# Kernel tuning notes

Measured on AMD Instinct MI355X. Metric: run time of the kernel, lower is better.

Reference implementation:

```python
import jax, jax.numpy as jnp
import numpy as np

HSIZE = 128
E = 640000


def _init_linear(key, fan_in, fan_out):
    # torch nn.Linear default init: U(-1/sqrt(fan_in), 1/sqrt(fan_in))
    kw, kb = jax.random.split(key)
    bound = 1.0 / np.sqrt(fan_in)
    W = jax.random.uniform(kw, (fan_in, fan_out), jnp.float32, -bound, bound)
    b = jax.random.uniform(kb, (fan_out,), jnp.float32, -bound, bound)
    return W, b


def setup_inputs() -> dict:
    key = jax.random.key(0)
    ks = jax.random.split(key, 6)
    hself = jax.random.normal(ks[0], (E, HSIZE), jnp.float32)
    hother = jax.random.normal(ks[1], (E, HSIZE), jnp.float32)
    Wm1, bm1 = _init_linear(ks[2], 2 * HSIZE, HSIZE)
    Wm2, bm2 = _init_linear(ks[3], HSIZE, HSIZE)
    Wu1, bu1 = _init_linear(ks[4], 2 * HSIZE, HSIZE)
    Wu2, bu2 = _init_linear(ks[5], HSIZE, HSIZE)
    return {"hself": hself, "hother": hother,
            "Wm1": Wm1, "bm1": bm1, "Wm2": Wm2, "bm2": bm2,
            "Wu1": Wu1, "bu1": bu1, "Wu2": Wu2, "bu2": bu2}


def _mlp2(a, b, W1, b1, W2, b2):
    # concat([a, b], -1) @ W1 done without materializing the concat
    h = a @ W1[:HSIZE] + b @ W1[HSIZE:] + b1
    h = jax.nn.relu(h)
    return h @ W2 + b2


def reference(hself, hother, Wm1, bm1, Wm2, bm2, Wu1, bu1, Wu2, bu2):
    # msg: Linear(2h,h) -> ReLU -> Linear(h,h) on cat([hself, hother])
    msg = _mlp2(hself, hother, Wm1, bm1, Wm2, bm2)
    # upd: Linear(2h,h) -> ReLU -> Linear(h,h) on cat([hself, msg])
    out = _mlp2(hself, msg, Wu1, bu1, Wu2, bu2)
    return out
```

## Files before the change

### kernel.cpp

```cpp
#include <hip/hip_runtime.h>

typedef __bf16 bf16_t;
typedef __bf16 bf16x8 __attribute__((ext_vector_type(8)));
typedef float f32x4 __attribute__((ext_vector_type(4)));

#define MFMA(a, b, c) __builtin_amdgcn_mfma_f32_16x16x32_bf16((a), (b), (c), 0, 0, 0)

#define E_ROWS 640000
#define BM 256

static __device__ __forceinline__ bf16x8 cvt8(float4 a, float4 b) {
  bf16x8 r;
  r[0] = (bf16_t)a.x; r[1] = (bf16_t)a.y; r[2] = (bf16_t)a.z; r[3] = (bf16_t)a.w;
  r[4] = (bf16_t)b.x; r[5] = (bf16_t)b.y; r[6] = (bf16_t)b.z; r[7] = (bf16_t)b.w;
  return r;
}

static __device__ __forceinline__ unsigned int pk2(float a, float b) {
  unsigned short ua = __builtin_bit_cast(unsigned short, (bf16_t)a);
  unsigned short ub = __builtin_bit_cast(unsigned short, (bf16_t)b);
  return ((unsigned int)ub << 16) | ua;
}

static __device__ __forceinline__ void gload_lds16(const void* g, void* l) {
  __builtin_amdgcn_global_load_lds(
      (const __attribute__((address_space(1))) unsigned int*)g,
      (__attribute__((address_space(3))) unsigned int*)l, 16, 0, 0);
}

__global__ __launch_bounds__(256) void prep_weights(
    const float* __restrict__ Wm1, const float* __restrict__ Wm2,
    const float* __restrict__ Wu1, const float* __restrict__ Wu2,
    bf16_t* __restrict__ wt) {
  int c = blockIdx.x * 256 + threadIdx.x;
  if (c >= 12288) return;
  int lane = c & 63, f = c >> 6;
  const float* W; int base;
  if (f < 64)       { W = Wm1; base = 0;   }
  else if (f < 96)  { W = Wm2; base = 64;  }
  else if (f < 160) { W = Wu1; base = 96;  }
  else              { W = Wu2; base = 160; }
  int fl = f - base;
  int ks = fl >> 3, nb = fl & 7;
  int k0 = 32 * ks + 8 * (lane >> 4);
  int n  = 16 * nb + (lane & 15);
  bf16x8 v;
  #pragma unroll
  for (int j = 0; j < 8; ++j) v[j] = (bf16_t)W[(size_t)(k0 + j) * 128 + n];
  ((bf16x8*)wt)[c] = v;
}

#define STAGE96(tc0) { \
  _Pragma("unroll") \
  for (int i_ = 0; i_ < 12; ++i_) \
    gload_lds16((const char*)wt + ((size_t)((tc0) + i_ * 512 + tid)) * 16, \
                smem + (i_ * 512 + tid) * 16); }

#define LDW8(s, base, fl0) \
  s##0 = *(const bf16x8*)((base) + ((fl0) + 0) * 1024 + lane * 16); \
  s##1 = *(const bf16x8*)((base) + ((fl0) + 1) * 1024 + lane * 16); \
  s##2 = *(const bf16x8*)((base) + ((fl0) + 2) * 1024 + lane * 16); \
  s##3 = *(const bf16x8*)((base) + ((fl0) + 3) * 1024 + lane * 16); \
  s##4 = *(const bf16x8*)((base) + ((fl0) + 4) * 1024 + lane * 16); \
  s##5 = *(const bf16x8*)((base) + ((fl0) + 5) * 1024 + lane * 16); \
  s##6 = *(const bf16x8*)((base) + ((fl0) + 6) * 1024 + lane * 16); \
  s##7 = *(const bf16x8*)((base) + ((fl0) + 7) * 1024 + lane * 16);

#define ROUND(s, x0, x1) \
  acc00 = MFMA(s##0, x0, acc00); acc10 = MFMA(s##0, x1, acc10); \
  acc01 = MFMA(s##1, x0, acc01); acc11 = MFMA(s##1, x1, acc11); \
  acc02 = MFMA(s##2, x0, acc02); acc12 = MFMA(s##2, x1, acc12); \
  acc03 = MFMA(s##3, x0, acc03); acc13 = MFMA(s##3, x1, acc13); \
  acc04 = MFMA(s##4, x0, acc04); acc14 = MFMA(s##4, x1, acc14); \
  acc05 = MFMA(s##5, x0, acc05); acc15 = MFMA(s##5, x1, acc15); \
  acc06 = MFMA(s##6, x0, acc06); acc16 = MFMA(s##6, x1, acc16); \
  acc07 = MFMA(s##7, x0, acc07); acc17 = MFMA(s##7, x1, acc17);

#define ACCINIT(bp) { const float* bp_ = (bp) + g * 4; float4 q; \
  q = *(const float4*)(bp_ +   0); acc00 = (f32x4){q.x,q.y,q.z,q.w}; acc10 = acc00; \
  q = *(const float4*)(bp_ +  16); acc01 = (f32x4){q.x,q.y,q.z,q.w}; acc11 = acc01; \
  q = *(const float4*)(bp_ +  32); acc02 = (f32x4){q.x,q.y,q.z,q.w}; acc12 = acc02; \
  q = *(const float4*)(bp_ +  48); acc03 = (f32x4){q.x,q.y,q.z,q.w}; acc13 = acc03; \
  q = *(const float4*)(bp_ +  64); acc04 = (f32x4){q.x,q.y,q.z,q.w}; acc14 = acc04; \
  q = *(const float4*)(bp_ +  80); acc05 = (f32x4){q.x,q.y,q.z,q.w}; acc15 = acc05; \
  q = *(const float4*)(bp_ +  96); acc06 = (f32x4){q.x,q.y,q.z,q.w}; acc16 = acc06; \
  q = *(const float4*)(bp_ + 112); acc07 = (f32x4){q.x,q.y,q.z,q.w}; acc17 = acc07; }

#define RPK_H(av, nb, R) { \
  f32x4 v = av; \
  float e0 = v[0], e1 = v[1], e2 = v[2], e3 = v[3]; \
  if (R) { e0 = fmaxf(e0, 0.f); e1 = fmaxf(e1, 0.f); \
           e2 = fmaxf(e2, 0.f); e3 = fmaxf(e3, 0.f); } \
  uint2 w; w.x = pk2(e0, e1); w.y = pk2(e2, e3); \
  int dl = c + 16 * (2 * ((nb) & 1) + (g >> 1)); \
  *(uint2*)(myrep + (((nb) >> 1) * 64 + dl) * 16 + (g & 1) * 8) = w; }

#define WAITLDS asm volatile("s_waitcnt lgkmcnt(0)" ::: "memory");
#define VMCNT0  asm volatile("s_waitcnt vmcnt(0)" ::: "memory");

#define REPACK(R) \
  RPK_H(acc00, 0, R) RPK_H(acc01, 1, R) RPK_H(acc02, 2, R) RPK_H(acc03, 3, R) \
  RPK_H(acc04, 4, R) RPK_H(acc05, 5, R) RPK_H(acc06, 6, R) RPK_H(acc07, 7, R) \
  WAITLDS \
  x00 = *(const bf16x8*)(myrep + (0 * 64 + lane) * 16); \
  x01 = *(const bf16x8*)(myrep + (1 * 64 + lane) * 16); \
  x02 = *(const bf16x8*)(myrep + (2 * 64 + lane) * 16); \
  x03 = *(const bf16x8*)(myrep + (3 * 64 + lane) * 16); \
  WAITLDS \
  RPK_H(acc10, 0, R) RPK_H(acc11, 1, R) RPK_H(acc12, 2, R) RPK_H(acc13, 3, R) \
  RPK_H(acc14, 4, R) RPK_H(acc15, 5, R) RPK_H(acc16, 6, R) RPK_H(acc17, 7, R) \
  WAITLDS \
  x10 = *(const bf16x8*)(myrep + (0 * 64 + lane) * 16); \
  x11 = *(const bf16x8*)(myrep + (1 * 64 + lane) * 16); \
  x12 = *(const bf16x8*)(myrep + (2 * 64 + lane) * 16); \
  x13 = *(const bf16x8*)(myrep + (3 * 64 + lane) * 16); \
  WAITLDS

#define LOADX(d0, d1, basep, kk) { \
  float4 a0 = *(const float4*)((basep) + r0 + (kk) * 32); \
  float4 a1 = *(const float4*)((basep) + r0 + (kk) * 32 + 4); \
  float4 b0 = *(const float4*)((basep) + r1 + (kk) * 32); \
  float4 b1 = *(const float4*)((basep) + r1 + (kk) * 32 + 4); \
  d0 = cvt8(a0, a1); d1 = cvt8(b0, b1); }

#define ST(av, mt, nb) { f32x4 v = av; \
  *(float4*)(out + (rowbase + (mt) * 16 + c) * 128 + (nb) * 16 + g * 4) = \
      (float4){v[0], v[1], v[2], v[3]}; }

__global__ __launch_bounds__(512) void fused_mp(
    const float* __restrict__ hself, const float* __restrict__ hother,
    const bf16_t* __restrict__ wt,
    const float* __restrict__ bm1, const float* __restrict__ bm2,
    const float* __restrict__ bu1, const float* __restrict__ bu2,
    float* __restrict__ out) {
  __shared__ char smem[131072];

  const int tid = threadIdx.x;
  const int lane = tid & 63;
  const int wave = tid >> 6;
  const int c = lane & 15;
  const int g = lane >> 4;

  char* W1 = smem;
  char* W2 = smem + 65536;
  char* myrep = smem + 98304 + wave * 4096;

  const size_t rowbase = (size_t)blockIdx.x * BM + wave * 32;
  const size_t r0 = (rowbase + c) * 128 + g * 8;
  const size_t r1 = (rowbase + 16 + c) * 128 + g * 8;

  bf16x8 hs00, hs01, hs02, hs03, hs10, hs11, hs12, hs13;
  bf16x8 x00, x01, x02, x03, x10, x11, x12, x13;
  LOADX(hs00, hs10, hself, 0)
  LOADX(hs01, hs11, hself, 1)
  LOADX(hs02, hs12, hself, 2)
  LOADX(hs03, hs13, hself, 3)
  STAGE96(0)
  LOADX(x00, x10, hother, 0)
  LOADX(x01, x11, hother, 1)
  LOADX(x02, x12, hother, 2)
  LOADX(x03, x13, hother, 3)
  VMCNT0
  __syncthreads();

  f32x4 acc00, acc01, acc02, acc03, acc04, acc05, acc06, acc07;
  f32x4 acc10, acc11, acc12, acc13, acc14, acc15, acc16, acc17;
  bf16x8 wa0, wa1, wa2, wa3, wa4, wa5, wa6, wa7;

  ACCINIT(bm1)
  LDW8(wa, W1, 0)   ROUND(wa, hs00, hs10)
  LDW8(wa, W1, 8)   ROUND(wa, hs01, hs11)
  LDW8(wa, W1, 16)  ROUND(wa, hs02, hs12)
  LDW8(wa, W1, 24)  ROUND(wa, hs03, hs13)
  LDW8(wa, W1, 32)  ROUND(wa, x00, x10)
  LDW8(wa, W1, 40)  ROUND(wa, x01, x11)
  LDW8(wa, W1, 48)  ROUND(wa, x02, x12)
  LDW8(wa, W1, 56)  ROUND(wa, x03, x13)

  REPACK(true)

  ACCINIT(bm2)
  LDW8(wa, W2, 0)   ROUND(wa, x00, x10)
  LDW8(wa, W2, 8)   ROUND(wa, x01, x11)
  LDW8(wa, W2, 16)  ROUND(wa, x02, x12)
  LDW8(wa, W2, 24)  ROUND(wa, x03, x13)

  REPACK(false)

  __syncthreads();
  STAGE96(6144)
  VMCNT0
  __syncthreads();

  ACCINIT(bu1)
  LDW8(wa, W1, 0)   ROUND(wa, hs00, hs10)
  LDW8(wa, W1, 8)   ROUND(wa, hs01, hs11)
  LDW8(wa, W1, 16)  ROUND(wa, hs02, hs12)
  LDW8(wa, W1, 24)  ROUND(wa, hs03, hs13)
  LDW8(wa, W1, 32)  ROUND(wa, x00, x10)
  LDW8(wa, W1, 40)  ROUND(wa, x01, x11)
  LDW8(wa, W1, 48)  ROUND(wa, x02, x12)
  LDW8(wa, W1, 56)  ROUND(wa, x03, x13)

  REPACK(true)

  ACCINIT(bu2)
  LDW8(wa, W2, 0)   ROUND(wa, x00, x10)
  LDW8(wa, W2, 8)   ROUND(wa, x01, x11)
  LDW8(wa, W2, 16)  ROUND(wa, x02, x12)
  LDW8(wa, W2, 24)  ROUND(wa, x03, x13)

  ST(acc00, 0, 0) ST(acc01, 0, 1) ST(acc02, 0, 2) ST(acc03, 0, 3)
  ST(acc04, 0, 4) ST(acc05, 0, 5) ST(acc06, 0, 6) ST(acc07, 0, 7)
  ST(acc10, 1, 0) ST(acc11, 1, 1) ST(acc12, 1, 2) ST(acc13, 1, 3)
  ST(acc14, 1, 4) ST(acc15, 1, 5) ST(acc16, 1, 6) ST(acc17, 1, 7)
}

extern "C" void kernel_launch(void* const* d_in, const int* in_sizes, int n_in,
                              void* d_out, int out_size, void* d_ws, size_t ws_size,
                              hipStream_t stream) {
  const float* hself  = (const float*)d_in[0];
  const float* hother = (const float*)d_in[1];
  const float* Wm1 = (const float*)d_in[2];
  const float* bm1 = (const float*)d_in[3];
  const float* Wm2 = (const float*)d_in[4];
  const float* bm2 = (const float*)d_in[5];
  const float* Wu1 = (const float*)d_in[6];
  const float* bu1 = (const float*)d_in[7];
  const float* Wu2 = (const float*)d_in[8];
  const float* bu2 = (const float*)d_in[9];
  float* out = (float*)d_out;
  bf16_t* wt = (bf16_t*)d_ws;

  prep_weights<<<48, 256, 0, stream>>>(Wm1, Wm2, Wu1, Wu2, wt);
  fused_mp<<<E_ROWS / BM, 512, 0, stream>>>(hself, hother, wt,
                                            bm1, bm2, bu1, bu2, out);
}
```

Before: 289.2 us.

## Make fused MLP kernel persistent with double-buffered prefetch of next tile

The kernel becomes persistent: 250 blocks each loop over 10 row tiles in two interleaved register sets (A/B). The next tile's hother and hself loads and the weight restaging are issued before the current tile's compute and waited on with partial vmcnt, so global latency can overlap MFMA work. This removes per-block launch and prologue costs, but it doubles input register pressure and issues a redundant final prefetch (tile index wraps to 0). With 250 blocks on a 256-CU part, load balance and occupancy may suffer.

```diff
diff --git a/kernel.cpp b/kernel.cpp
--- a/kernel.cpp
+++ b/kernel.cpp
@@ -8,6 +8,8 @@
 
 #define E_ROWS 640000
 #define BM 256
+#define NTILE 2500
+#define GRID 250
 
 static __device__ __forceinline__ bf16x8 cvt8(float4 a, float4 b) {
   bf16x8 r;
@@ -97,35 +99,81 @@
 
 #define WAITLDS asm volatile("s_waitcnt lgkmcnt(0)" ::: "memory");
 #define VMCNT0  asm volatile("s_waitcnt vmcnt(0)" ::: "memory");
-
-#define REPACK(R) \
+#define VMCNT16 asm volatile("s_waitcnt vmcnt(16)" ::: "memory");
+
+#define REPACK(R, x) \
   RPK_H(acc00, 0, R) RPK_H(acc01, 1, R) RPK_H(acc02, 2, R) RPK_H(acc03, 3, R) \
   RPK_H(acc04, 4, R) RPK_H(acc05, 5, R) RPK_H(acc06, 6, R) RPK_H(acc07, 7, R) \
   WAITLDS \
-  x00 = *(const bf16x8*)(myrep + (0 * 64 + lane) * 16); \
-  x01 = *(const bf16x8*)(myrep + (1 * 64 + lane) * 16); \
-  x02 = *(const bf16x8*)(myrep + (2 * 64 + lane) * 16); \
-  x03 = *(const bf16x8*)(myrep + (3 * 64 + lane) * 16); \
+  x##00 = *(const bf16x8*)(myrep + (0 * 64 + lane) * 16); \
+  x##01 = *(const bf16x8*)(myrep + (1 * 64 + lane) * 16); \
+  x##02 = *(const bf16x8*)(myrep + (2 * 64 + lane) * 16); \
+  x##03 = *(const bf16x8*)(myrep + (3 * 64 + lane) * 16); \
   WAITLDS \
   RPK_H(acc10, 0, R) RPK_H(acc11, 1, R) RPK_H(acc12, 2, R) RPK_H(acc13, 3, R) \
   RPK_H(acc14, 4, R) RPK_H(acc15, 5, R) RPK_H(acc16, 6, R) RPK_H(acc17, 7, R) \
   WAITLDS \
-  x10 = *(const bf16x8*)(myrep + (0 * 64 + lane) * 16); \
-  x11 = *(const bf16x8*)(myrep + (1 * 64 + lane) * 16); \
-  x12 = *(const bf16x8*)(myrep + (2 * 64 + lane) * 16); \
-  x13 = *(const bf16x8*)(myrep + (3 * 64 + lane) * 16); \
+  x##10 = *(const bf16x8*)(myrep + (0 * 64 + lane) * 16); \
+  x##11 = *(const bf16x8*)(myrep + (1 * 64 + lane) * 16); \
+  x##12 = *(const bf16x8*)(myrep + (2 * 64 + lane) * 16); \
+  x##13 = *(const bf16x8*)(myrep + (3 * 64 + lane) * 16); \
   WAITLDS
 
-#define LOADX(d0, d1, basep, kk) { \
-  float4 a0 = *(const float4*)((basep) + r0 + (kk) * 32); \
-  float4 a1 = *(const float4*)((basep) + r0 + (kk) * 32 + 4); \
-  float4 b0 = *(const float4*)((basep) + r1 + (kk) * 32); \
-  float4 b1 = *(const float4*)((basep) + r1 + (kk) * 32 + 4); \
+#define LOADX(d0, d1, basep, kk, rr0, rr1) { \
+  float4 a0 = *(const float4*)((basep) + (rr0) + (kk) * 32); \
+  float4 a1 = *(const float4*)((basep) + (rr0) + (kk) * 32 + 4); \
+  float4 b0 = *(const float4*)((basep) + (rr1) + (kk) * 32); \
+  float4 b1 = *(const float4*)((basep) + (rr1) + (kk) * 32 + 4); \
   d0 = cvt8(a0, a1); d1 = cvt8(b0, b1); }
 
-#define ST(av, mt, nb) { f32x4 v = av; \
-  *(float4*)(out + (rowbase + (mt) * 16 + c) * 128 + (nb) * 16 + g * 4) = \
+#define LOADX4(pfx, basep, rr0, rr1) \
+  LOADX(pfx##00, pfx##10, basep, 0, rr0, rr1) \
+  LOADX(pfx##01, pfx##11, basep, 1, rr0, rr1) \
+  LOADX(pfx##02, pfx##12, basep, 2, rr0, rr1) \
+  LOADX(pfx##03, pfx##13, basep, 3, rr0, rr1)
+
+#define ST(av, mt, nb, rb) { f32x4 v = av; \
+  *(float4*)(out + ((rb) + (mt) * 16 + c) * 128 + (nb) * 16 + g * 4) = \
       (float4){v[0], v[1], v[2], v[3]}; }
+
+#define FIRST_HALF(hs, x) \
+  ACCINIT(bm1) \
+  LDW8(wa, W1, 0)   ROUND(wa, hs##00, hs##10) \
+  LDW8(wa, W1, 8)   ROUND(wa, hs##01, hs##11) \
+  LDW8(wa, W1, 16)  ROUND(wa, hs##02, hs##12) \
+  LDW8(wa, W1, 24)  ROUND(wa, hs##03, hs##13) \
+  LDW8(wa, W1, 32)  ROUND(wa, x##00, x##10) \
+  LDW8(wa, W1, 40)  ROUND(wa, x##01, x##11) \
+  LDW8(wa, W1, 48)  ROUND(wa, x##02, x##12) \
+  LDW8(wa, W1, 56)  ROUND(wa, x##03, x##13) \
+  REPACK(true, x) \
+  ACCINIT(bm2) \
+  LDW8(wa, W2, 0)   ROUND(wa, x##00, x##10) \
+  LDW8(wa, W2, 8)   ROUND(wa, x##01, x##11) \
+  LDW8(wa, W2, 16)  ROUND(wa, x##02, x##12) \
+  LDW8(wa, W2, 24)  ROUND(wa, x##03, x##13) \
+  REPACK(false, x)
+
+#define SECOND_HALF(hs, x, rb) \
+  ACCINIT(bu1) \
+  LDW8(wa, W1, 0)   ROUND(wa, hs##00, hs##10) \
+  LDW8(wa, W1, 8)   ROUND(wa, hs##01, hs##11) \
+  LDW8(wa, W1, 16)  ROUND(wa, hs##02, hs##12) \
+  LDW8(wa, W1, 24)  ROUND(wa, hs##03, hs##13) \
+  LDW8(wa, W1, 32)  ROUND(wa, x##00, x##10) \
+  LDW8(wa, W1, 40)  ROUND(wa, x##01, x##11) \
+  LDW8(wa, W1, 48)  ROUND(wa, x##02, x##12) \
+  LDW8(wa, W1, 56)  ROUND(wa, x##03, x##13) \
+  REPACK(true, x) \
+  ACCINIT(bu2) \
+  LDW8(wa, W2, 0)   ROUND(wa, x##00, x##10) \
+  LDW8(wa, W2, 8)   ROUND(wa, x##01, x##11) \
+  LDW8(wa, W2, 16)  ROUND(wa, x##02, x##12) \
+  LDW8(wa, W2, 24)  ROUND(wa, x##03, x##13) \
+  ST(acc00, 0, 0, rb) ST(acc01, 0, 1, rb) ST(acc02, 0, 2, rb) ST(acc03, 0, 3, rb) \
+  ST(acc04, 0, 4, rb) ST(acc05, 0, 5, rb) ST(acc06, 0, 6, rb) ST(acc07, 0, 7, rb) \
+  ST(acc10, 1, 0, rb) ST(acc11, 1, 1, rb) ST(acc12, 1, 2, rb) ST(acc13, 1, 3, rb) \
+  ST(acc14, 1, 4, rb) ST(acc15, 1, 5, rb) ST(acc16, 1, 6, rb) ST(acc17, 1, 7, rb)
 
 __global__ __launch_bounds__(512) void fused_mp(
     const float* __restrict__ hself, const float* __restrict__ hother,
@@ -145,75 +193,65 @@
   char* W2 = smem + 65536;
   char* myrep = smem + 98304 + wave * 4096;
 
-  const size_t rowbase = (size_t)blockIdx.x * BM + wave * 32;
-  const size_t r0 = (rowbase + c) * 128 + g * 8;
-  const size_t r1 = (rowbase + 16 + c) * 128 + g * 8;
-
-  bf16x8 hs00, hs01, hs02, hs03, hs10, hs11, hs12, hs13;
-  bf16x8 x00, x01, x02, x03, x10, x11, x12, x13;
-  LOADX(hs00, hs10, hself, 0)
-  LOADX(hs01, hs11, hself, 1)
-  LOADX(hs02, hs12, hself, 2)
-  LOADX(hs03, hs13, hself, 3)
-  STAGE96(0)
-  LOADX(x00, x10, hother, 0)
-  LOADX(x01, x11, hother, 1)
-  LOADX(x02, x12, hother, 2)
-  LOADX(x03, x13, hother, 3)
-  VMCNT0
-  __syncthreads();
-
+  bf16x8 hsA00, hsA01, hsA02, hsA03, hsA10, hsA11, hsA12, hsA13;
+  bf16x8 xA00, xA01, xA02, xA03, xA10, xA11, xA12, xA13;
+  bf16x8 hsB00, hsB01, hsB02, hsB03, hsB10, hsB11, hsB12, hsB13;
+  bf16x8 xB00, xB01, xB02, xB03, xB10, xB11, xB12, xB13;
   f32x4 acc00, acc01, acc02, acc03, acc04, acc05, acc06, acc07;
   f32x4 acc10, acc11, acc12, acc13, acc14, acc15, acc16, acc17;
   bf16x8 wa0, wa1, wa2, wa3, wa4, wa5, wa6, wa7;
 
-  ACCINIT(bm1)
-  LDW8(wa, W1, 0)   ROUND(wa, hs00, hs10)
-  LDW8(wa, W1, 8)   ROUND(wa, hs01, hs11)
-  LDW8(wa, W1, 16)  ROUND(wa, hs02, hs12)
-  LDW8(wa, W1, 24)  ROUND(wa, hs03, hs13)
-  LDW8(wa, W1, 32)  ROUND(wa, x00, x10)
-  LDW8(wa, W1, 40)  ROUND(wa, x01, x11)
-  LDW8(wa, W1, 48)  ROUND(wa, x02, x12)
-  LDW8(wa, W1, 56)  ROUND(wa, x03, x13)
-
-  REPACK(true)
-
-  ACCINIT(bm2)
-  LDW8(wa, W2, 0)   ROUND(wa, x00, x10)
-  LDW8(wa, W2, 8)   ROUND(wa, x01, x11)
-  LDW8(wa, W2, 16)  ROUND(wa, x02, x12)
-  LDW8(wa, W2, 24)  ROUND(wa, x03, x13)
-
-  REPACK(false)
-
-  __syncthreads();
-  STAGE96(6144)
-  VMCNT0
-  __syncthreads();
-
-  ACCINIT(bu1)
-  LDW8(wa, W1, 0)   ROUND(wa, hs00, hs10)
-  LDW8(wa, W1, 8)   ROUND(wa, hs01, hs11)
-  LDW8(wa, W1, 16)  ROUND(wa, hs02, hs12)
-  LDW8(wa, W1, 24)  ROUND(wa, hs03, hs13)
-  LDW8(wa, W1, 32)  ROUND(wa, x00, x10)
-  LDW8(wa, W1, 40)  ROUND(wa, x01, x11)
-  LDW8(wa, W1, 48)  ROUND(wa, x02, x12)
-  LDW8(wa, W1, 56)  ROUND(wa, x03, x13)
-
-  REPACK(true)
-
-  ACCINIT(bu2)
-  LDW8(wa, W2, 0)   ROUND(wa, x00, x10)
-  LDW8(wa, W2, 8)   ROUND(wa, x01, x11)
-  LDW8(wa, W2, 16)  ROUND(wa, x02, x12)
-  LDW8(wa, W2, 24)  ROUND(wa, x03, x13)
-
-  ST(acc00, 0, 0) ST(acc01, 0, 1) ST(acc02, 0, 2) ST(acc03, 0, 3)
-  ST(acc04, 0, 4) ST(acc05, 0, 5) ST(acc06, 0, 6) ST(acc07, 0, 7)
-  ST(acc10, 1, 0) ST(acc11, 1, 1) ST(acc12, 1, 2) ST(acc13, 1, 3)
-  ST(acc14, 1, 4) ST(acc15, 1, 5) ST(acc16, 1, 6) ST(acc17, 1, 7)
+  {
+    STAGE96(0)
+    __builtin_amdgcn_sched_barrier(0);
+    size_t rb = (size_t)blockIdx.x * BM + wave * 32;
+    size_t rr0 = (rb + c) * 128 + g * 8, rr1 = rr0 + 2048;
+    LOADX4(hsA, hself, rr0, rr1)
+    LOADX4(xA, hother, rr0, rr1)
+    VMCNT0
+    __syncthreads();
+  }
+
+  #pragma unroll 1
+  for (int it = 0; it < 5; ++it) {
+    const int tA = blockIdx.x + it * 500;
+    const int tB = tA + 250;
+    int tN = tA + 500; if (tN >= NTILE) tN = 0;
+
+    const size_t rbA = (size_t)tA * BM + wave * 32;
+    const size_t rbB = (size_t)tB * BM + wave * 32;
+    const size_t rbN = (size_t)tN * BM + wave * 32;
+    const size_t r0B = (rbB + c) * 128 + g * 8, r1B = r0B + 2048;
+    const size_t r0N = (rbN + c) * 128 + g * 8, r1N = r0N + 2048;
+
+    FIRST_HALF(hsA, xA)
+    __syncthreads();
+    STAGE96(6144)
+    __builtin_amdgcn_sched_barrier(0);
+    LOADX4(xB, hother, r0B, r1B)
+    VMCNT16
+    __syncthreads();
+    SECOND_HALF(hsA, xA, rbA)
+    __syncthreads();
+    LOADX4(hsB, hself, r0B, r1B)
+    STAGE96(0)
+    VMCNT0
+    __syncthreads();
+
+    FIRST_HALF(hsB, xB)
+    __syncthreads();
+    STAGE96(6144)
+    __builtin_amdgcn_sched_barrier(0);
+    LOADX4(xA, hother, r0N, r1N)
+    VMCNT16
+    __syncthreads();
+    SECOND_HALF(hsB, xB, rbB)
+    __syncthreads();
+    LOADX4(hsA, hself, r0N, r1N)
+    STAGE96(0)
+    VMCNT0
+    __syncthreads();
+  }
 }
 
 extern "C" void kernel_launch(void* const* d_in, const int* in_sizes, int n_in,
@@ -233,6 +271,6 @@
   bf16_t* wt = (bf16_t*)d_ws;
 
   prep_weights<<<48, 256, 0, stream>>>(Wm1, Wm2, Wu1, Wu2, wt);
-  fused_mp<<<E_ROWS / BM, 512, 0, stream>>>(hself, hother, wt,
-                                            bm1, bm2, bu1, bu2, out);
-}
+  fused_mp<<<GRID, 512, 0, stream>>>(hself, hother, wt,
+                                     bm1, bm2, bu1, bu2, out);
+}
```

New measurement: 345.0 us. +19.3%, slower.

## Halve block size and stage one weight matrix at a time for two blocks per CU

Applied to the files above, without the earlier changes.

Shrinks blocks from 512 to 256 threads (128 rows each) and cuts LDS from 128KB to 80KB by staging only one layer's weights at a time. Each layer's weights are reloaded into the same buffer while the REPACK step runs, with extra barriers. The aim is two resident blocks per CU, so one block's weight staging and global loads overlap another block's compute. In exchange, weight traffic into LDS per row doubles and each block has more syncs.

```diff
diff --git a/kernel.cpp b/kernel.cpp
--- a/kernel.cpp
+++ b/kernel.cpp
@@ -7,7 +7,7 @@
 #define MFMA(a, b, c) __builtin_amdgcn_mfma_f32_16x16x32_bf16((a), (b), (c), 0, 0, 0)
 
 #define E_ROWS 640000
-#define BM 256
+#define BM 128
 
 static __device__ __forceinline__ bf16x8 cvt8(float4 a, float4 b) {
   bf16x8 r;
@@ -50,21 +50,26 @@
   ((bf16x8*)wt)[c] = v;
 }
 
-#define STAGE96(tc0) { \
+#define STAGE64(tc0) { \
   _Pragma("unroll") \
-  for (int i_ = 0; i_ < 12; ++i_) \
-    gload_lds16((const char*)wt + ((size_t)((tc0) + i_ * 512 + tid)) * 16, \
-                smem + (i_ * 512 + tid) * 16); }
-
-#define LDW8(s, base, fl0) \
-  s##0 = *(const bf16x8*)((base) + ((fl0) + 0) * 1024 + lane * 16); \
-  s##1 = *(const bf16x8*)((base) + ((fl0) + 1) * 1024 + lane * 16); \
-  s##2 = *(const bf16x8*)((base) + ((fl0) + 2) * 1024 + lane * 16); \
-  s##3 = *(const bf16x8*)((base) + ((fl0) + 3) * 1024 + lane * 16); \
-  s##4 = *(const bf16x8*)((base) + ((fl0) + 4) * 1024 + lane * 16); \
-  s##5 = *(const bf16x8*)((base) + ((fl0) + 5) * 1024 + lane * 16); \
-  s##6 = *(const bf16x8*)((base) + ((fl0) + 6) * 1024 + lane * 16); \
-  s##7 = *(const bf16x8*)((base) + ((fl0) + 7) * 1024 + lane * 16);
+  for (int i_ = 0; i_ < 16; ++i_) \
+    gload_lds16((const char*)wt + ((size_t)((tc0) + i_ * 256 + tid)) * 16, \
+                smem + (i_ * 256 + tid) * 16); }
+#define STAGE32(tc0) { \
+  _Pragma("unroll") \
+  for (int i_ = 0; i_ < 8; ++i_) \
+    gload_lds16((const char*)wt + ((size_t)((tc0) + i_ * 256 + tid)) * 16, \
+                smem + (i_ * 256 + tid) * 16); }
+
+#define LDW8(s, fl0) \
+  s##0 = *(const bf16x8*)(smem + ((fl0) + 0) * 1024 + lane * 16); \
+  s##1 = *(const bf16x8*)(smem + ((fl0) + 1) * 1024 + lane * 16); \
+  s##2 = *(const bf16x8*)(smem + ((fl0) + 2) * 1024 + lane * 16); \
+  s##3 = *(const bf16x8*)(smem + ((fl0) + 3) * 1024 + lane * 16); \
+  s##4 = *(const bf16x8*)(smem + ((fl0) + 4) * 1024 + lane * 16); \
+  s##5 = *(const bf16x8*)(smem + ((fl0) + 5) * 1024 + lane * 16); \
+  s##6 = *(const bf16x8*)(smem + ((fl0) + 6) * 1024 + lane * 16); \
+  s##7 = *(const bf16x8*)(smem + ((fl0) + 7) * 1024 + lane * 16);
 
 #define ROUND(s, x0, x1) \
   acc00 = MFMA(s##0, x0, acc00); acc10 = MFMA(s##0, x1, acc10); \
@@ -127,13 +132,13 @@
   *(float4*)(out + (rowbase + (mt) * 16 + c) * 128 + (nb) * 16 + g * 4) = \
       (float4){v[0], v[1], v[2], v[3]}; }
 
-__global__ __launch_bounds__(512) void fused_mp(
+__global__ __launch_bounds__(256, 2) void fused_mp(
     const float* __restrict__ hself, const float* __restrict__ hother,
     const bf16_t* __restrict__ wt,
     const float* __restrict__ bm1, const float* __restrict__ bm2,
     const float* __restrict__ bu1, const float* __restrict__ bu2,
     float* __restrict__ out) {
-  __shared__ char smem[131072];
+  __shared__ char smem[81920];
 
   const int tid = threadIdx.x;
   const int lane = tid & 63;
@@ -141,9 +146,7 @@
   const int c = lane & 15;
   const int g = lane >> 4;
 
-  char* W1 = smem;
-  char* W2 = smem + 65536;
-  char* myrep = smem + 98304 + wave * 4096;
+  char* myrep = smem + 65536 + wave * 4096;
 
   const size_t rowbase = (size_t)blockIdx.x * BM + wave * 32;
   const size_t r0 = (rowbase + c) * 128 + g * 8;
@@ -151,11 +154,12 @@
 
   bf16x8 hs00, hs01, hs02, hs03, hs10, hs11, hs12, hs13;
   bf16x8 x00, x01, x02, x03, x10, x11, x12, x13;
+  STAGE64(0)
+  __builtin_amdgcn_sched_barrier(0);
   LOADX(hs00, hs10, hself, 0)
   LOADX(hs01, hs11, hself, 1)
   LOADX(hs02, hs12, hself, 2)
   LOADX(hs03, hs13, hself, 3)
-  STAGE96(0)
   LOADX(x00, x10, hother, 0)
   LOADX(x01, x11, hother, 1)
   LOADX(x02, x12, hother, 2)
@@ -168,47 +172,54 @@
   bf16x8 wa0, wa1, wa2, wa3, wa4, wa5, wa6, wa7;
 
   ACCINIT(bm1)
-  LDW8(wa, W1, 0)   ROUND(wa, hs00, hs10)
-  LDW8(wa, W1, 8)   ROUND(wa, hs01, hs11)
-  LDW8(wa, W1, 16)  ROUND(wa, hs02, hs12)
-  LDW8(wa, W1, 24)  ROUND(wa, hs03, hs13)
-  LDW8(wa, W1, 32)  ROUND(wa, x00, x10)
-  LDW8(wa, W1, 40)  ROUND(wa, x01, x11)
-  LDW8(wa, W1, 48)  ROUND(wa, x02, x12)
-  LDW8(wa, W1, 56)  ROUND(wa, x03, x13)
-
+  LDW8(wa, 0)   ROUND(wa, hs00, hs10)
+  LDW8(wa, 8)   ROUND(wa, hs01, hs11)
+  LDW8(wa, 16)  ROUND(wa, hs02, hs12)
+  LDW8(wa, 24)  ROUND(wa, hs03, hs13)
+  LDW8(wa, 32)  ROUND(wa, x00, x10)
+  LDW8(wa, 40)  ROUND(wa, x01, x11)
+  LDW8(wa, 48)  ROUND(wa, x02, x12)
+  LDW8(wa, 56)  ROUND(wa, x03, x13)
+  __syncthreads();
+
+  STAGE32(4096)
   REPACK(true)
+  VMCNT0
+  __syncthreads();
 
   ACCINIT(bm2)
-  LDW8(wa, W2, 0)   ROUND(wa, x00, x10)
-  LDW8(wa, W2, 8)   ROUND(wa, x01, x11)
-  LDW8(wa, W2, 16)  ROUND(wa, x02, x12)
-  LDW8(wa, W2, 24)  ROUND(wa, x03, x13)
-
+  LDW8(wa, 0)   ROUND(wa, x00, x10)
+  LDW8(wa, 8)   ROUND(wa, x01, x11)
+  LDW8(wa, 16)  ROUND(wa, x02, x12)
+  LDW8(wa, 24)  ROUND(wa, x03, x13)
+  __syncthreads();
+
+  STAGE64(6144)
   REPACK(false)
-
-  __syncthreads();
-  STAGE96(6144)
   VMCNT0
   __syncthreads();
 
   ACCINIT(bu1)
-  LDW8(wa, W1, 0)   ROUND(wa, hs00, hs10)
-  LDW8(wa, W1, 8)   ROUND(wa, hs01, hs11)
-  LDW8(wa, W1, 16)  ROUND(wa, hs02, hs12)
-  LDW8(wa, W1, 24)  ROUND(wa, hs03, hs13)
-  LDW8(wa, W1, 32)  ROUND(wa, x00, x10)
-  LDW8(wa, W1, 40)  ROUND(wa, x01, x11)
-  LDW8(wa, W1, 48)  ROUND(wa, x02, x12)
-  LDW8(wa, W1, 56)  ROUND(wa, x03, x13)
-
+  LDW8(wa, 0)   ROUND(wa, hs00, hs10)
+  LDW8(wa, 8)   ROUND(wa, hs01, hs11)
+  LDW8(wa, 16)  ROUND(wa, hs02, hs12)
+  LDW8(wa, 24)  ROUND(wa, hs03, hs13)
+  LDW8(wa, 32)  ROUND(wa, x00, x10)
+  LDW8(wa, 40)  ROUND(wa, x01, x11)
+  LDW8(wa, 48)  ROUND(wa, x02, x12)
+  LDW8(wa, 56)  ROUND(wa, x03, x13)
+  __syncthreads();
+
+  STAGE32(10240)
   REPACK(true)
+  VMCNT0
+  __syncthreads();
 
   ACCINIT(bu2)
-  LDW8(wa, W2, 0)   ROUND(wa, x00, x10)
-  LDW8(wa, W2, 8)   ROUND(wa, x01, x11)
-  LDW8(wa, W2, 16)  ROUND(wa, x02, x12)
-  LDW8(wa, W2, 24)  ROUND(wa, x03, x13)
+  LDW8(wa, 0)   ROUND(wa, x00, x10)
+  LDW8(wa, 8)   ROUND(wa, x01, x11)
+  LDW8(wa, 16)  ROUND(wa, x02, x12)
+  LDW8(wa, 24)  ROUND(wa, x03, x13)
 
   ST(acc00, 0, 0) ST(acc01, 0, 1) ST(acc02, 0, 2) ST(acc03, 0, 3)
   ST(acc04, 0, 4) ST(acc05, 0, 5) ST(acc06, 0, 6) ST(acc07, 0, 7)
@@ -233,6 +244,6 @@
   bf16_t* wt = (bf16_t*)d_ws;
 
   prep_weights<<<48, 256, 0, stream>>>(Wm1, Wm2, Wu1, Wu2, wt);
-  fused_mp<<<E_ROWS / BM, 512, 0, stream>>>(hself, hother, wt,
+  fused_mp<<<E_ROWS / BM, 256, 0, stream>>>(hself, hother, wt,
                                             bm1, bm2, bu1, bu2, out);
 }
```

Measured after the change: 760.5 us. 163% more time.

## Halve rows per block and stream weights through two 32KB LDS buffers

Applied to the files above, without the earlier changes.

Each wave now processes 16 rows instead of 32, so a block covers 128 rows. Weights are no longer held as a 96KB stage plus a repack area. They stream through two 32KB LDS halves (LO/UP) in 32KB chunks, and the repack scratch reuses whichever half is free. This cuts LDS use from 128KB to 64KB per block and halves accumulator registers, which should allow two blocks per CU and better latency hiding. The cost is twice as many blocks, each re-staging all weights, and more barriers per block.

```diff
diff --git a/kernel.cpp b/kernel.cpp
--- a/kernel.cpp
+++ b/kernel.cpp
@@ -7,7 +7,7 @@
 #define MFMA(a, b, c) __builtin_amdgcn_mfma_f32_16x16x32_bf16((a), (b), (c), 0, 0, 0)
 
 #define E_ROWS 640000
-#define BM 256
+#define BM 128
 
 static __device__ __forceinline__ bf16x8 cvt8(float4 a, float4 b) {
   bf16x8 r;
@@ -50,11 +50,16 @@
   ((bf16x8*)wt)[c] = v;
 }
 
-#define STAGE96(tc0) { \
+#define STAGE64(tc0) { \
   _Pragma("unroll") \
-  for (int i_ = 0; i_ < 12; ++i_) \
+  for (int i_ = 0; i_ < 8; ++i_) \
     gload_lds16((const char*)wt + ((size_t)((tc0) + i_ * 512 + tid)) * 16, \
                 smem + (i_ * 512 + tid) * 16); }
+#define STAGE32(tc0, dst) { \
+  _Pragma("unroll") \
+  for (int i_ = 0; i_ < 4; ++i_) \
+    gload_lds16((const char*)wt + ((size_t)((tc0) + i_ * 512 + tid)) * 16, \
+                (dst) + (i_ * 512 + tid) * 16); }
 
 #define LDW8(s, base, fl0) \
   s##0 = *(const bf16x8*)((base) + ((fl0) + 0) * 1024 + lane * 16); \
@@ -66,65 +71,52 @@
   s##6 = *(const bf16x8*)((base) + ((fl0) + 6) * 1024 + lane * 16); \
   s##7 = *(const bf16x8*)((base) + ((fl0) + 7) * 1024 + lane * 16);
 
-#define ROUND(s, x0, x1) \
-  acc00 = MFMA(s##0, x0, acc00); acc10 = MFMA(s##0, x1, acc10); \
-  acc01 = MFMA(s##1, x0, acc01); acc11 = MFMA(s##1, x1, acc11); \
-  acc02 = MFMA(s##2, x0, acc02); acc12 = MFMA(s##2, x1, acc12); \
-  acc03 = MFMA(s##3, x0, acc03); acc13 = MFMA(s##3, x1, acc13); \
-  acc04 = MFMA(s##4, x0, acc04); acc14 = MFMA(s##4, x1, acc14); \
-  acc05 = MFMA(s##5, x0, acc05); acc15 = MFMA(s##5, x1, acc15); \
-  acc06 = MFMA(s##6, x0, acc06); acc16 = MFMA(s##6, x1, acc16); \
-  acc07 = MFMA(s##7, x0, acc07); acc17 = MFMA(s##7, x1, acc17);
+#define ROUND(s, x0) \
+  acc0 = MFMA(s##0, x0, acc0); acc1 = MFMA(s##1, x0, acc1); \
+  acc2 = MFMA(s##2, x0, acc2); acc3 = MFMA(s##3, x0, acc3); \
+  acc4 = MFMA(s##4, x0, acc4); acc5 = MFMA(s##5, x0, acc5); \
+  acc6 = MFMA(s##6, x0, acc6); acc7 = MFMA(s##7, x0, acc7);
 
 #define ACCINIT(bp) { const float* bp_ = (bp) + g * 4; float4 q; \
-  q = *(const float4*)(bp_ +   0); acc00 = (f32x4){q.x,q.y,q.z,q.w}; acc10 = acc00; \
-  q = *(const float4*)(bp_ +  16); acc01 = (f32x4){q.x,q.y,q.z,q.w}; acc11 = acc01; \
-  q = *(const float4*)(bp_ +  32); acc02 = (f32x4){q.x,q.y,q.z,q.w}; acc12 = acc02; \
-  q = *(const float4*)(bp_ +  48); acc03 = (f32x4){q.x,q.y,q.z,q.w}; acc13 = acc03; \
-  q = *(const float4*)(bp_ +  64); acc04 = (f32x4){q.x,q.y,q.z,q.w}; acc14 = acc04; \
-  q = *(const float4*)(bp_ +  80); acc05 = (f32x4){q.x,q.y,q.z,q.w}; acc15 = acc05; \
-  q = *(const float4*)(bp_ +  96); acc06 = (f32x4){q.x,q.y,q.z,q.w}; acc16 = acc06; \
-  q = *(const float4*)(bp_ + 112); acc07 = (f32x4){q.x,q.y,q.z,q.w}; acc17 = acc07; }
-
-#define RPK_H(av, nb, R) { \
+  q = *(const float4*)(bp_ +   0); acc0 = (f32x4){q.x,q.y,q.z,q.w}; \
+  q = *(const float4*)(bp_ +  16); acc1 = (f32x4){q.x,q.y,q.z,q.w}; \
+  q = *(const float4*)(bp_ +  32); acc2 = (f32x4){q.x,q.y,q.z,q.w}; \
+  q = *(const float4*)(bp_ +  48); acc3 = (f32x4){q.x,q.y,q.z,q.w}; \
+  q = *(const float4*)(bp_ +  64); acc4 = (f32x4){q.x,q.y,q.z,q.w}; \
+  q = *(const float4*)(bp_ +  80); acc5 = (f32x4){q.x,q.y,q.z,q.w}; \
+  q = *(const float4*)(bp_ +  96); acc6 = (f32x4){q.x,q.y,q.z,q.w}; \
+  q = *(const float4*)(bp_ + 112); acc7 = (f32x4){q.x,q.y,q.z,q.w}; }
+
+#define RPK(av, nb, R) { \
   f32x4 v = av; \
   float e0 = v[0], e1 = v[1], e2 = v[2], e3 = v[3]; \
   if (R) { e0 = fmaxf(e0, 0.f); e1 = fmaxf(e1, 0.f); \
            e2 = fmaxf(e2, 0.f); e3 = fmaxf(e3, 0.f); } \
   uint2 w; w.x = pk2(e0, e1); w.y = pk2(e2, e3); \
   int dl = c + 16 * (2 * ((nb) & 1) + (g >> 1)); \
-  *(uint2*)(myrep + (((nb) >> 1) * 64 + dl) * 16 + (g & 1) * 8) = w; }
+  *(uint2*)((myrep) + (((nb) >> 1) * 64 + dl) * 16 + (g & 1) * 8) = w; }
 
 #define WAITLDS asm volatile("s_waitcnt lgkmcnt(0)" ::: "memory");
 #define VMCNT0  asm volatile("s_waitcnt vmcnt(0)" ::: "memory");
 
-#define REPACK(R) \
-  RPK_H(acc00, 0, R) RPK_H(acc01, 1, R) RPK_H(acc02, 2, R) RPK_H(acc03, 3, R) \
-  RPK_H(acc04, 4, R) RPK_H(acc05, 5, R) RPK_H(acc06, 6, R) RPK_H(acc07, 7, R) \
+#define REPACK(R, rbase) { \
+  char* myrep = (rbase) + wave * 4096; \
+  RPK(acc0, 0, R) RPK(acc1, 1, R) RPK(acc2, 2, R) RPK(acc3, 3, R) \
+  RPK(acc4, 4, R) RPK(acc5, 5, R) RPK(acc6, 6, R) RPK(acc7, 7, R) \
   WAITLDS \
-  x00 = *(const bf16x8*)(myrep + (0 * 64 + lane) * 16); \
-  x01 = *(const bf16x8*)(myrep + (1 * 64 + lane) * 16); \
-  x02 = *(const bf16x8*)(myrep + (2 * 64 + lane) * 16); \
-  x03 = *(const bf16x8*)(myrep + (3 * 64 + lane) * 16); \
-  WAITLDS \
-  RPK_H(acc10, 0, R) RPK_H(acc11, 1, R) RPK_H(acc12, 2, R) RPK_H(acc13, 3, R) \
-  RPK_H(acc14, 4, R) RPK_H(acc15, 5, R) RPK_H(acc16, 6, R) RPK_H(acc17, 7, R) \
-  WAITLDS \
-  x10 = *(const bf16x8*)(myrep + (0 * 64 + lane) * 16); \
-  x11 = *(const bf16x8*)(myrep + (1 * 64 + lane) * 16); \
-  x12 = *(const bf16x8*)(myrep + (2 * 64 + lane) * 16); \
-  x13 = *(const bf16x8*)(myrep + (3 * 64 + lane) * 16); \
-  WAITLDS
-
-#define LOADX(d0, d1, basep, kk) { \
+  x0 = *(const bf16x8*)(myrep + (0 * 64 + lane) * 16); \
+  x1 = *(const bf16x8*)(myrep + (1 * 64 + lane) * 16); \
+  x2 = *(const bf16x8*)(myrep + (2 * 64 + lane) * 16); \
+  x3 = *(const bf16x8*)(myrep + (3 * 64 + lane) * 16); \
+  WAITLDS }
+
+#define LOADX(d0, basep, kk) { \
   float4 a0 = *(const float4*)((basep) + r0 + (kk) * 32); \
   float4 a1 = *(const float4*)((basep) + r0 + (kk) * 32 + 4); \
-  float4 b0 = *(const float4*)((basep) + r1 + (kk) * 32); \
-  float4 b1 = *(const float4*)((basep) + r1 + (kk) * 32 + 4); \
-  d0 = cvt8(a0, a1); d1 = cvt8(b0, b1); }
-
-#define ST(av, mt, nb) { f32x4 v = av; \
-  *(float4*)(out + (rowbase + (mt) * 16 + c) * 128 + (nb) * 16 + g * 4) = \
+  d0 = cvt8(a0, a1); }
+
+#define ST(av, nb) { f32x4 v = av; \
+  *(float4*)(out + (rowbase + c) * 128 + (nb) * 16 + g * 4) = \
       (float4){v[0], v[1], v[2], v[3]}; }
 
 __global__ __launch_bounds__(512) void fused_mp(
@@ -133,7 +125,7 @@
     const float* __restrict__ bm1, const float* __restrict__ bm2,
     const float* __restrict__ bu1, const float* __restrict__ bu2,
     float* __restrict__ out) {
-  __shared__ char smem[131072];
+  __shared__ char smem[65536];
 
   const int tid = threadIdx.x;
   const int lane = tid & 63;
@@ -141,79 +133,85 @@
   const int c = lane & 15;
   const int g = lane >> 4;
 
-  char* W1 = smem;
-  char* W2 = smem + 65536;
-  char* myrep = smem + 98304 + wave * 4096;
-
-  const size_t rowbase = (size_t)blockIdx.x * BM + wave * 32;
+  char* LO = smem;
+  char* UP = smem + 32768;
+
+  const size_t rowbase = (size_t)blockIdx.x * BM + wave * 16;
   const size_t r0 = (rowbase + c) * 128 + g * 8;
-  const size_t r1 = (rowbase + 16 + c) * 128 + g * 8;
-
-  bf16x8 hs00, hs01, hs02, hs03, hs10, hs11, hs12, hs13;
-  bf16x8 x00, x01, x02, x03, x10, x11, x12, x13;
-  LOADX(hs00, hs10, hself, 0)
-  LOADX(hs01, hs11, hself, 1)
-  LOADX(hs02, hs12, hself, 2)
-  LOADX(hs03, hs13, hself, 3)
-  STAGE96(0)
-  LOADX(x00, x10, hother, 0)
-  LOADX(x01, x11, hother, 1)
-  LOADX(x02, x12, hother, 2)
-  LOADX(x03, x13, hother, 3)
-  VMCNT0
-  __syncthreads();
-
-  f32x4 acc00, acc01, acc02, acc03, acc04, acc05, acc06, acc07;
-  f32x4 acc10, acc11, acc12, acc13, acc14, acc15, acc16, acc17;
+
+  bf16x8 hs0, hs1, hs2, hs3;
+  bf16x8 x0, x1, x2, x3;
+  STAGE64(0)
+  __builtin_amdgcn_sched_barrier(0);
+  LOADX(hs0, hself, 0)
+  LOADX(hs1, hself, 1)
+  LOADX(hs2, hself, 2)
+  LOADX(hs3, hself, 3)
+  LOADX(x0, hother, 0)
+  LOADX(x1, hother, 1)
+  LOADX(x2, hother, 2)
+  LOADX(x3, hother, 3)
+  VMCNT0
+  __syncthreads();
+
+  f32x4 acc0, acc1, acc2, acc3, acc4, acc5, acc6, acc7;
   bf16x8 wa0, wa1, wa2, wa3, wa4, wa5, wa6, wa7;
 
   ACCINIT(bm1)
-  LDW8(wa, W1, 0)   ROUND(wa, hs00, hs10)
-  LDW8(wa, W1, 8)   ROUND(wa, hs01, hs11)
-  LDW8(wa, W1, 16)  ROUND(wa, hs02, hs12)
-  LDW8(wa, W1, 24)  ROUND(wa, hs03, hs13)
-  LDW8(wa, W1, 32)  ROUND(wa, x00, x10)
-  LDW8(wa, W1, 40)  ROUND(wa, x01, x11)
-  LDW8(wa, W1, 48)  ROUND(wa, x02, x12)
-  LDW8(wa, W1, 56)  ROUND(wa, x03, x13)
-
-  REPACK(true)
+  LDW8(wa, LO, 0)   ROUND(wa, hs0)
+  LDW8(wa, LO, 8)   ROUND(wa, hs1)
+  LDW8(wa, LO, 16)  ROUND(wa, hs2)
+  LDW8(wa, LO, 24)  ROUND(wa, hs3)
+  LDW8(wa, UP, 0)   ROUND(wa, x0)
+  LDW8(wa, UP, 8)   ROUND(wa, x1)
+  LDW8(wa, UP, 16)  ROUND(wa, x2)
+  LDW8(wa, UP, 24)  ROUND(wa, x3)
+  __syncthreads();
+
+  STAGE32(4096, UP)
+  REPACK(true, LO)
+  VMCNT0
+  __syncthreads();
 
   ACCINIT(bm2)
-  LDW8(wa, W2, 0)   ROUND(wa, x00, x10)
-  LDW8(wa, W2, 8)   ROUND(wa, x01, x11)
-  LDW8(wa, W2, 16)  ROUND(wa, x02, x12)
-  LDW8(wa, W2, 24)  ROUND(wa, x03, x13)
-
-  REPACK(false)
-
-  __syncthreads();
-  STAGE96(6144)
-  VMCNT0
-  __syncthreads();
-
+  LDW8(wa, UP, 0)   ROUND(wa, x0)
+  LDW8(wa, UP, 8)   ROUND(wa, x1)
+  LDW8(wa, UP, 16)  ROUND(wa, x2)
+  LDW8(wa, UP, 24)  ROUND(wa, x3)
+  __syncthreads();
+
+  STAGE32(6144, LO)
+  REPACK(false, UP)
+  VMCNT0
+  __syncthreads();
+
+  STAGE32(8192, UP)
   ACCINIT(bu1)
-  LDW8(wa, W1, 0)   ROUND(wa, hs00, hs10)
-  LDW8(wa, W1, 8)   ROUND(wa, hs01, hs11)
-  LDW8(wa, W1, 16)  ROUND(wa, hs02, hs12)
-  LDW8(wa, W1, 24)  ROUND(wa, hs03, hs13)
-  LDW8(wa, W1, 32)  ROUND(wa, x00, x10)
-  LDW8(wa, W1, 40)  ROUND(wa, x01, x11)
-  LDW8(wa, W1, 48)  ROUND(wa, x02, x12)
-  LDW8(wa, W1, 56)  ROUND(wa, x03, x13)
-
-  REPACK(true)
+  LDW8(wa, LO, 0)   ROUND(wa, hs0)
+  LDW8(wa, LO, 8)   ROUND(wa, hs1)
+  LDW8(wa, LO, 16)  ROUND(wa, hs2)
+  LDW8(wa, LO, 24)  ROUND(wa, hs3)
+  VMCNT0
+  __syncthreads();
+  LDW8(wa, UP, 0)   ROUND(wa, x0)
+  LDW8(wa, UP, 8)   ROUND(wa, x1)
+  LDW8(wa, UP, 16)  ROUND(wa, x2)
+  LDW8(wa, UP, 24)  ROUND(wa, x3)
+  __syncthreads();
+
+  STAGE32(10240, LO)
+  REPACK(true, UP)
+  VMCNT0
+  __syncthreads();
 
   ACCINIT(bu2)
-  LDW8(wa, W2, 0)   ROUND(wa, x00, x10)
-  LDW8(wa, W2, 8)   ROUND(wa, x01, x11)
-  LDW8(wa, W2, 16)  ROUND(wa, x02, x12)
-  LDW8(wa, W2, 24)  ROUND(wa, x03, x13)
-
-  ST(acc00, 0, 0) ST(acc01, 0, 1) ST(acc02, 0, 2) ST(acc03, 0, 3)
-  ST(acc04, 0, 4) ST(acc05, 0, 5) ST(acc06, 0, 6) ST(acc07, 0, 7)
-  ST(acc10, 1, 0) ST(acc11, 1, 1) ST(acc12, 1, 2) ST(acc13, 1, 3)
-  ST(acc14, 1, 4) ST(acc15, 1, 5) ST(acc16, 1, 6) ST(acc17, 1, 7)
+  LDW8(wa, LO, 0)   ROUND(wa, x0)
+  LDW8(wa, LO, 8)   ROUND(wa, x1)
+  LDW8(wa, LO, 16)  ROUND(wa, x2)
+  LDW8(wa, LO, 24)  ROUND(wa, x3)
+
+  ST(acc0, 0) ST(acc1, 1) ST(acc2, 2) ST(acc3, 3)
+  ST(acc4, 4) ST(acc5, 5) ST(acc6, 6) ST(acc7, 7)
 }
 
 extern "C" void kernel_launch(void* const* d_in, const int* in_sizes, int n_in,
```

New measurement: 337.8 us. +16.8%, slower.
